# Kernel optimization log

Measured on AMD Instinct MI355X. Metric: run time of the kernel, lower is better.

## Reference

```python
import jax, jax.numpy as jnp
import numpy as np
import math

SEQ_LEN, PRED_LEN, CHANNELS, RANK = 720, 336, 862, 32
IN_LEN = SEQ_LEN // 2  # Haar low-pass with stride 2 (seq_len even)
BATCH = 256


def _dct2_ortho_mat(N):
    # D[k, n] = s_k * 2 * cos(pi * k * (2n+1) / (2N)); orthonormal DCT-II
    k = np.arange(N)[:, None]
    n = np.arange(N)[None, :]
    D = 2.0 * np.cos(np.pi * k * (2 * n + 1) / (2 * N))
    s = np.full(N, np.sqrt(1.0 / (2 * N)))
    s[0] = np.sqrt(1.0 / (4 * N))
    return jnp.asarray((s[:, None] * D).astype(np.float32))


def _idct2_unnorm_mat(N):
    # scipy.fft.idct(type=2, norm=None): out[n] = (1/N) * (x0/2 + sum_{k>=1} x_k cos(pi k (2n+1)/(2N)))
    # Returned as M[k, n] so that out = x @ M along last axis.
    k = np.arange(N)[:, None]
    n = np.arange(N)[None, :]
    M = np.cos(np.pi * k * (2 * n + 1) / (2 * N)) / N
    M[0, :] *= 0.5
    return jnp.asarray(M.astype(np.float32))


D_DCT = _dct2_ortho_mat(IN_LEN)        # [IN_LEN, IN_LEN]
M_IDCT = _idct2_unnorm_mat(PRED_LEN)   # [PRED_LEN, PRED_LEN]
INV_SQRT2 = 1.0 / math.sqrt(2.0)


def setup_inputs() -> dict:
    key = jax.random.key(0)
    k1, k2, k3, k4 = jax.random.split(key, 4)
    x = jax.random.normal(k1, (BATCH, SEQ_LEN, CHANNELS), dtype=jnp.float32)
    # kaiming_uniform-like scales for LowRank params
    boundA = math.sqrt(6.0 / IN_LEN)
    boundB = math.sqrt(6.0 / RANK)
    A = jax.random.uniform(k2, (IN_LEN, RANK), dtype=jnp.float32, minval=-boundA, maxval=boundA)
    B = jax.random.uniform(k3, (RANK, PRED_LEN), dtype=jnp.float32, minval=-boundB, maxval=boundB)
    b = jax.random.uniform(k4, (PRED_LEN,), dtype=jnp.float32)
    return {"x": x, "A": A, "B": B, "b": b}


def reference(x, A, B, b):
    # x: [B, L, C] -> [B, C, L]
    xt = jnp.transpose(x, (0, 2, 1))
    seq_mean = jnp.mean(xt, axis=-1, keepdims=True)          # [B, C, 1]
    xc = xt - seq_mean
    # Haar low-pass: depthwise conv1d with [1,1]/sqrt(2), stride 2
    h = (xc[..., ::2] + xc[..., 1::2]) * INV_SQRT2           # [B, C, IN_LEN]
    # orthonormal DCT-II along last axis, then divide by length
    y = jnp.einsum('bcn,kn->bck', h, D_DCT) / IN_LEN         # [B, C, IN_LEN]
    # low-rank prediction head (shared across channels)
    z = (y @ A) @ B + b                                      # [B, C, PRED_LEN]
    # unnormalized inverse DCT-II (scipy idct type=2, norm=None)
    o = z @ M_IDCT                                           # [B, C, PRED_LEN]
    o = o + seq_mean
    return jnp.transpose(o, (0, 2, 1))                       # [B, PRED_LEN, C]
```

## Files before the change

kernel.cpp:

```cpp
#include <hip/hip_runtime.h>
#include <math.h>

#define SEQ_LEN   720
#define IN_LEN    360
#define PRED_LEN  336
#define CHANNELS  862
#define RANK      32
#define BATCH     256

typedef _Float16 h2 __attribute__((ext_vector_type(2)));

#define WS_WP    0
#define WS_VT    11520
#define WS_CVEC  22272
#define WS_WH    22608
#define WS_VH    28368

__device__ __forceinline__ float fdot2w(h2 a, h2 b, float c) {
#if __has_builtin(__builtin_amdgcn_fdot2)
    return __builtin_amdgcn_fdot2(a, b, c, false);
#else
    return fmaf((float)a[0], (float)b[0], fmaf((float)a[1], (float)b[1], c));
#endif
}
__device__ __forceinline__ h2 pkrtz(float a, float b) {
    return __builtin_bit_cast(h2, __builtin_amdgcn_cvt_pkrtz(a, b));
}
#define BC(u) __builtin_bit_cast(h2, (u))

__global__ __launch_bounds__(256) void k_prep(const float* __restrict__ A,
                                              const float* __restrict__ B,
                                              const float* __restrict__ bias,
                                              float* __restrict__ Wp,
                                              float* __restrict__ Vt,
                                              float* __restrict__ cvec) {
    __shared__ float sbuf[IN_LEN * RANK];
    int blk = blockIdx.x;
    if (blk < 45) {
        for (int i = threadIdx.x; i < IN_LEN * RANK; i += 256) sbuf[i] = A[i];
        __syncthreads();
        int idx = blk * 256 + threadIdx.x;
        int n = idx >> 5, r = idx & 31;
        int step = 2 * n + 1, m = 0;
        float sum = 0.f;
        for (int k = 0; k < IN_LEN; ++k) {
            float coef = (k == 0) ? 0.05270462766947299f
                                  : 0.07453559924999299f;
            float d = coef * cospif((float)m * (1.0f / 720.0f));
            sum = fmaf(d, sbuf[k * RANK + r], sum);
            m += step; if (m >= 1440) m -= 1440;
        }
        Wp[idx] = sum * 0.0019641855032960957f;
    } else if (blk < 87) {
        for (int i = threadIdx.x; i < PRED_LEN * RANK; i += 256) {
            int r = i / PRED_LEN, k = i - r * PRED_LEN;
            sbuf[k * RANK + r] = B[i];
        }
        __syncthreads();
        int idx = (blk - 45) * 256 + threadIdx.x;
        int n = idx >> 5, r = idx & 31;
        int step = 2 * n + 1, m = 0;
        float sum = 0.f;
        for (int k = 0; k < PRED_LEN; ++k) {
            float mk = cospif((float)m * (1.0f / 672.0f));
            if (k == 0) mk *= 0.5f;
            sum = fmaf(mk, sbuf[k * RANK + r], sum);
            m += step; if (m >= 1344) m -= 1344;
        }
        Vt[idx] = sum * (1.0f / 336.0f);
    } else {
        int n = (blk - 87) * 256 + threadIdx.x;
        if (n < PRED_LEN) {
            int step = 2 * n + 1, m = 0;
            float sum = 0.f;
            for (int k = 0; k < PRED_LEN; ++k) {
                float mk = cospif((float)m * (1.0f / 672.0f));
                if (k == 0) mk *= 0.5f;
                sum = fmaf(mk, bias[k], sum);
                m += step; if (m >= 1344) m -= 1344;
            }
            cvec[n] = sum * (1.0f / 336.0f);
        }
    }
}

__global__ __launch_bounds__(256) void k_pack(const float* __restrict__ Wp,
                                              const float* __restrict__ Vt,
                                              unsigned* __restrict__ Wh,
                                              unsigned* __restrict__ Vh) {
    int idx = blockIdx.x * 256 + threadIdx.x;
    if (idx < 5760) {
        int np = idx >> 5, r = idx & 31;
        h2 v = pkrtz(Wp[(2 * np) * RANK + r], Wp[(2 * np + 1) * RANK + r]);
        Wh[idx] = __builtin_bit_cast(unsigned, v);
    } else if (idx < 5760 + 5376) {
        int j = idx - 5760;
        int n = j >> 4, q = j & 15;
        h2 v = pkrtz(Vt[n * RANK + 2 * q], Vt[n * RANK + 2 * q + 1]);
        Vh[j] = __builtin_bit_cast(unsigned, v);
    }
}

__global__ __launch_bounds__(448) void k_main(const float* __restrict__ x,
                                              const float* __restrict__ A,
                                              const unsigned* __restrict__ Wh,
                                              const unsigned* __restrict__ Vh,
                                              const float* __restrict__ cvec,
                                              float* __restrict__ out) {
    __shared__ uint4 lds4[2868];
    unsigned* ldsu = (unsigned*)lds4;
    const int tid = threadIdx.x;
    const int b = blockIdx.x;
    const int c0 = 2 * tid;
    const bool active = (tid < 431);

    for (int i = tid; i < 1440; i += 448) lds4[i] = ((const uint4*)Wh)[i];
    for (int i = tid; i < 1344; i += 448) lds4[1440 + i] = ((const uint4*)Vh)[i];
    for (int i = tid; i < PRED_LEN; i += 448) ldsu[11136 + i] = __float_as_uint(cvec[i]);
    __syncthreads();

    float acc0[RANK], acc1[RANK];
    #pragma unroll
    for (int r = 0; r < RANK; ++r) { acc0[r] = 0.f; acc1[r] = 0.f; }
    float S0 = 0.f, S1 = 0.f, mean0 = 0.f, mean1 = 0.f;
    h2 th0[16], th1[16];

    if (active) {
        const float* xp = x + (size_t)b * (SEQ_LEN * CHANNELS) + c0;

        float2 bufA[8], bufB[8];
        #define LOADB(BUF, BD) { const float* p_ = xp + (size_t)(BD) * (8 * CHANNELS); \
            _Pragma("unroll") \
            for (int j_ = 0; j_ < 8; ++j_) BUF[j_] = *(const float2*)(p_ + j_ * CHANNELS); }

        #define NPBODY(BUF, S_) { \
            float pe0 = BUF[4*S_+0].x + BUF[4*S_+1].x; \
            float pe1 = BUF[4*S_+0].y + BUF[4*S_+1].y; \
            float po0 = BUF[4*S_+2].x + BUF[4*S_+3].x; \
            float po1 = BUF[4*S_+2].y + BUF[4*S_+3].y; \
            S0 += pe0 + po0; S1 += pe1 + po1; \
            h2 P0 = pkrtz(pe0, po0); \
            h2 P1 = pkrtz(pe1, po1); \
            _Pragma("unroll") \
            for (int q_ = 0; q_ < 8; ++q_) { \
                uint4 wv = wr[8*S_ + q_]; \
                acc0[4*q_+0] = fdot2w(P0, BC(wv.x), acc0[4*q_+0]); \
                acc1[4*q_+0] = fdot2w(P1, BC(wv.x), acc1[4*q_+0]); \
                acc0[4*q_+1] = fdot2w(P0, BC(wv.y), acc0[4*q_+1]); \
                acc1[4*q_+1] = fdot2w(P1, BC(wv.y), acc1[4*q_+1]); \
                acc0[4*q_+2] = fdot2w(P0, BC(wv.z), acc0[4*q_+2]); \
                acc1[4*q_+2] = fdot2w(P1, BC(wv.z), acc1[4*q_+2]); \
                acc0[4*q_+3] = fdot2w(P0, BC(wv.w), acc0[4*q_+3]); \
                acc1[4*q_+3] = fdot2w(P1, BC(wv.w), acc1[4*q_+3]); \
            } }

        #define BODY(BUF, BD) { const uint4* wr = lds4 + 16 * (BD); \
            NPBODY(BUF, 0); NPBODY(BUF, 1); }

        LOADB(bufA, 0)
        for (int it = 0; it < 45; ++it) {
            LOADB(bufB, 2 * it + 1)
            BODY(bufA, 2 * it)
            if (it < 44) LOADB(bufA, 2 * it + 2)
            BODY(bufB, 2 * it + 1)
        }
        #undef BODY
        #undef NPBODY
        #undef LOADB

        const float k360 = (1.0f / 360.0f) * 0.037267799624996496f;
        float g0 = -S0 * k360, g1 = -S1 * k360;
        #pragma unroll
        for (int q = 0; q < 8; ++q) {
            float4 a4 = ((const float4*)A)[q];
            acc0[4*q+0] = fmaf(g0, a4.x, acc0[4*q+0]);
            acc1[4*q+0] = fmaf(g1, a4.x, acc1[4*q+0]);
            acc0[4*q+1] = fmaf(g0, a4.y, acc0[4*q+1]);
            acc1[4*q+1] = fmaf(g1, a4.y, acc1[4*q+1]);
            acc0[4*q+2] = fmaf(g0, a4.z, acc0[4*q+2]);
            acc1[4*q+2] = fmaf(g1, a4.z, acc1[4*q+2]);
            acc0[4*q+3] = fmaf(g0, a4.w, acc0[4*q+3]);
            acc1[4*q+3] = fmaf(g1, a4.w, acc1[4*q+3]);
        }
        mean0 = S0 * (1.0f / 720.0f);
        mean1 = S1 * (1.0f / 720.0f);

        #pragma unroll
        for (int u = 0; u < 16; ++u) {
            th0[u] = pkrtz(acc0[2*u], acc0[2*u+1]);
            th1[u] = pkrtz(acc1[2*u], acc1[2*u+1]);
        }

        float* op = out + (size_t)b * (PRED_LEN * CHANNELS) + c0;
        #pragma unroll 2
        for (int n = 0; n < PRED_LEN; ++n) {
            const uint4* vr = lds4 + 1440 + n * 4;
            float oA0 = 0.f, oB0 = 0.f, oA1 = 0.f, oB1 = 0.f;
            #pragma unroll
            for (int q = 0; q < 4; ++q) {
                uint4 v = vr[q];
                oA0 = fdot2w(th0[4*q+0], BC(v.x), oA0);
                oA1 = fdot2w(th1[4*q+0], BC(v.x), oA1);
                oB0 = fdot2w(th0[4*q+1], BC(v.y), oB0);
                oB1 = fdot2w(th1[4*q+1], BC(v.y), oB1);
                oA0 = fdot2w(th0[4*q+2], BC(v.z), oA0);
                oA1 = fdot2w(th1[4*q+2], BC(v.z), oA1);
                oB0 = fdot2w(th0[4*q+3], BC(v.w), oB0);
                oB1 = fdot2w(th1[4*q+3], BC(v.w), oB1);
            }
            float cvn = __uint_as_float(ldsu[11136 + n]);
            float2 o;
            o.x = (oA0 + oB0) + cvn + mean0;
            o.y = (oA1 + oB1) + cvn + mean1;
            *(float2*)op = o;
            op += CHANNELS;
        }
    }
}


extern "C" void kernel_launch(void* const* d_in, const int* in_sizes, int n_in,
                              void* d_out, int out_size, void* d_ws, size_t ws_size,
                              hipStream_t stream) {
    (void)in_sizes; (void)n_in; (void)out_size; (void)ws_size;
    const float* x    = (const float*)d_in[0];
    const float* A    = (const float*)d_in[1];
    const float* B    = (const float*)d_in[2];
    const float* bias = (const float*)d_in[3];
    float* out = (float*)d_out;
    float* ws  = (float*)d_ws;

    float*    Wp   = ws + WS_WP;
    float*    Vt   = ws + WS_VT;
    float*    cvec = ws + WS_CVEC;
    unsigned* Wh   = (unsigned*)(ws + WS_WH);
    unsigned* Vh   = (unsigned*)(ws + WS_VH);

    k_prep<<<dim3(89), dim3(256), 0, stream>>>(A, B, bias, Wp, Vt, cvec);
    k_pack<<<dim3(44), dim3(256), 0, stream>>>(Wp, Vt, Wh, Vh);
    k_main<<<dim3(BATCH), dim3(448), 0, stream>>>(x, A, Wh, Vh, cvec, out);
}
```

Before: 290.2 us.

## Split main kernel into sequence-half partial and prediction-half final kernels

Replaces the single per-batch kernel with two kernels. The first splits the sequence into two halves per batch, accumulating low-rank projections in packed fp16 FMA, and writes partial results and sums to workspace. The second combines the halves and computes the output for half of the prediction rows per block. This doubles the grid size, which should raise occupancy on a GPU that had only 256 blocks. In exchange it adds a workspace round-trip and an extra launch, and accumulating in fp16 instead of fp32 dot products reduces precision.

```diff
diff --git a/kernel.cpp b/kernel.cpp
--- a/kernel.cpp
+++ b/kernel.cpp
@@ -15,6 +15,8 @@
 #define WS_CVEC  22272
 #define WS_WH    22608
 #define WS_VH    28368
+#define WS_T     33744
+#define WS_S     7095248
 
 __device__ __forceinline__ float fdot2w(h2 a, h2 b, float c) {
 #if __has_builtin(__builtin_amdgcn_fdot2)
@@ -26,7 +28,8 @@
 __device__ __forceinline__ h2 pkrtz(float a, float b) {
     return __builtin_bit_cast(h2, __builtin_amdgcn_cvt_pkrtz(a, b));
 }
-#define BC(u) __builtin_bit_cast(h2, (u))
+#define BC(u)  __builtin_bit_cast(h2, (u))
+#define BCU(v) __builtin_bit_cast(unsigned, (v))
 
 __global__ __launch_bounds__(256) void k_prep(const float* __restrict__ A,
                                               const float* __restrict__ B,
@@ -90,131 +93,170 @@
                                               unsigned* __restrict__ Vh) {
     int idx = blockIdx.x * 256 + threadIdx.x;
     if (idx < 5760) {
-        int np = idx >> 5, r = idx & 31;
-        h2 v = pkrtz(Wp[(2 * np) * RANK + r], Wp[(2 * np + 1) * RANK + r]);
-        Wh[idx] = __builtin_bit_cast(unsigned, v);
+        int n = idx >> 4, j = idx & 15;
+        h2 v = pkrtz(Wp[n * RANK + 2 * j], Wp[n * RANK + 2 * j + 1]);
+        Wh[idx] = BCU(v);
     } else if (idx < 5760 + 5376) {
-        int j = idx - 5760;
-        int n = j >> 4, q = j & 15;
-        h2 v = pkrtz(Vt[n * RANK + 2 * q], Vt[n * RANK + 2 * q + 1]);
-        Vh[j] = __builtin_bit_cast(unsigned, v);
-    }
-}
-
-__global__ __launch_bounds__(448) void k_main(const float* __restrict__ x,
-                                              const float* __restrict__ A,
+        int k = idx - 5760;
+        int n = k >> 4, j = k & 15;
+        h2 v = pkrtz(Vt[n * RANK + 2 * j], Vt[n * RANK + 2 * j + 1]);
+        Vh[k] = BCU(v);
+    }
+}
+
+__global__ __launch_bounds__(512) void k_part(const float* __restrict__ x,
                                               const unsigned* __restrict__ Wh,
-                                              const unsigned* __restrict__ Vh,
-                                              const float* __restrict__ cvec,
-                                              float* __restrict__ out) {
-    __shared__ uint4 lds4[2868];
-    unsigned* ldsu = (unsigned*)lds4;
+                                              unsigned* __restrict__ wsT,
+                                              float* __restrict__ wsS) {
+    __shared__ uint4 lw4[720];
     const int tid = threadIdx.x;
-    const int b = blockIdx.x;
+    const int kh = blockIdx.x;
+    const int b  = blockIdx.y;
+
+    for (int i = tid; i < 720; i += 512)
+        lw4[i] = ((const uint4*)Wh)[kh * 720 + i];
+    __syncthreads();
+
     const int c0 = 2 * tid;
-    const bool active = (tid < 431);
-
-    for (int i = tid; i < 1440; i += 448) lds4[i] = ((const uint4*)Wh)[i];
-    for (int i = tid; i < 1344; i += 448) lds4[1440 + i] = ((const uint4*)Vh)[i];
-    for (int i = tid; i < PRED_LEN; i += 448) ldsu[11136 + i] = __float_as_uint(cvec[i]);
+    if (c0 >= CHANNELS) return;
+
+    h2 acc0[16], acc1[16];
+    #pragma unroll
+    for (int j = 0; j < 16; ++j) { acc0[j] = pkrtz(0.f, 0.f); acc1[j] = pkrtz(0.f, 0.f); }
+    float S0 = 0.f, S1 = 0.f;
+
+    const float* xp = x + (size_t)b * (SEQ_LEN * CHANNELS)
+                        + (size_t)kh * (IN_LEN * CHANNELS) + c0;
+
+    float2 bufA[8], bufB[8];
+    #define LOADB(BUF, CH) { const float* p_ = xp + (size_t)(CH) * (8 * CHANNELS); \
+        _Pragma("unroll") \
+        for (int j_ = 0; j_ < 8; ++j_) BUF[j_] = *(const float2*)(p_ + j_ * CHANNELS); }
+
+    #define BODY1(E, O, NL) { \
+        float p0 = E.x + O.x, p1 = E.y + O.y; \
+        S0 += p0; S1 += p1; \
+        h2 P0 = pkrtz(p0, p0), P1 = pkrtz(p1, p1); \
+        const uint4* wr = lw4 + (NL) * 4; \
+        _Pragma("unroll") \
+        for (int q_ = 0; q_ < 4; ++q_) { \
+            uint4 wv = wr[q_]; \
+            h2 w0 = BC(wv.x), w1 = BC(wv.y), w2 = BC(wv.z), w3 = BC(wv.w); \
+            acc0[4*q_+0] = w0 * P0 + acc0[4*q_+0]; \
+            acc1[4*q_+0] = w0 * P1 + acc1[4*q_+0]; \
+            acc0[4*q_+1] = w1 * P0 + acc0[4*q_+1]; \
+            acc1[4*q_+1] = w1 * P1 + acc1[4*q_+1]; \
+            acc0[4*q_+2] = w2 * P0 + acc0[4*q_+2]; \
+            acc1[4*q_+2] = w2 * P1 + acc1[4*q_+2]; \
+            acc0[4*q_+3] = w3 * P0 + acc0[4*q_+3]; \
+            acc1[4*q_+3] = w3 * P1 + acc1[4*q_+3]; \
+        } }
+
+    #define BODY4(BUF, NB) { \
+        BODY1(BUF[0], BUF[1], (NB) + 0) \
+        BODY1(BUF[2], BUF[3], (NB) + 1) \
+        BODY1(BUF[4], BUF[5], (NB) + 2) \
+        BODY1(BUF[6], BUF[7], (NB) + 3) }
+
+    LOADB(bufA, 0)
+    for (int it = 0; it < 22; ++it) {
+        LOADB(bufB, 2 * it + 1)
+        BODY4(bufA, 8 * it)
+        LOADB(bufA, 2 * it + 2)
+        BODY4(bufB, 8 * it + 4)
+    }
+    BODY4(bufA, 176)
+    #undef BODY4
+    #undef BODY1
+    #undef LOADB
+
+    uint4* r4 = (uint4*)(wsT + ((size_t)(kh * BATCH + b) * CHANNELS + c0) * 16);
+    #pragma unroll
+    for (int q = 0; q < 4; ++q) {
+        uint4 v;
+        v.x = BCU(acc0[4*q+0]); v.y = BCU(acc0[4*q+1]);
+        v.z = BCU(acc0[4*q+2]); v.w = BCU(acc0[4*q+3]);
+        r4[q] = v;
+        v.x = BCU(acc1[4*q+0]); v.y = BCU(acc1[4*q+1]);
+        v.z = BCU(acc1[4*q+2]); v.w = BCU(acc1[4*q+3]);
+        r4[4 + q] = v;
+    }
+    float2 sv; sv.x = S0; sv.y = S1;
+    *(float2*)(wsS + (size_t)(kh * BATCH + b) * CHANNELS + c0) = sv;
+}
+
+__global__ __launch_bounds__(512) void k_final(const float* __restrict__ A,
+                                               const unsigned* __restrict__ Vh,
+                                               const float* __restrict__ cvec,
+                                               const unsigned* __restrict__ wsT,
+                                               const float* __restrict__ wsS,
+                                               float* __restrict__ out) {
+    __shared__ uint4 lv4[672];
+    __shared__ float lcv[168];
+    const int tid = threadIdx.x;
+    const int nh = blockIdx.x;
+    const int b  = blockIdx.y;
+
+    for (int i = tid; i < 672; i += 512) lv4[i] = ((const uint4*)Vh)[nh * 672 + i];
+    for (int i = tid; i < 168; i += 512) lcv[i] = cvec[nh * 168 + i];
     __syncthreads();
 
-    float acc0[RANK], acc1[RANK];
-    #pragma unroll
-    for (int r = 0; r < RANK; ++r) { acc0[r] = 0.f; acc1[r] = 0.f; }
-    float S0 = 0.f, S1 = 0.f, mean0 = 0.f, mean1 = 0.f;
-    h2 th0[16], th1[16];
-
-    if (active) {
-        const float* xp = x + (size_t)b * (SEQ_LEN * CHANNELS) + c0;
-
-        float2 bufA[8], bufB[8];
-        #define LOADB(BUF, BD) { const float* p_ = xp + (size_t)(BD) * (8 * CHANNELS); \
-            _Pragma("unroll") \
-            for (int j_ = 0; j_ < 8; ++j_) BUF[j_] = *(const float2*)(p_ + j_ * CHANNELS); }
-
-        #define NPBODY(BUF, S_) { \
-            float pe0 = BUF[4*S_+0].x + BUF[4*S_+1].x; \
-            float pe1 = BUF[4*S_+0].y + BUF[4*S_+1].y; \
-            float po0 = BUF[4*S_+2].x + BUF[4*S_+3].x; \
-            float po1 = BUF[4*S_+2].y + BUF[4*S_+3].y; \
-            S0 += pe0 + po0; S1 += pe1 + po1; \
-            h2 P0 = pkrtz(pe0, po0); \
-            h2 P1 = pkrtz(pe1, po1); \
-            _Pragma("unroll") \
-            for (int q_ = 0; q_ < 8; ++q_) { \
-                uint4 wv = wr[8*S_ + q_]; \
-                acc0[4*q_+0] = fdot2w(P0, BC(wv.x), acc0[4*q_+0]); \
-                acc1[4*q_+0] = fdot2w(P1, BC(wv.x), acc1[4*q_+0]); \
-                acc0[4*q_+1] = fdot2w(P0, BC(wv.y), acc0[4*q_+1]); \
-                acc1[4*q_+1] = fdot2w(P1, BC(wv.y), acc1[4*q_+1]); \
-                acc0[4*q_+2] = fdot2w(P0, BC(wv.z), acc0[4*q_+2]); \
-                acc1[4*q_+2] = fdot2w(P1, BC(wv.z), acc1[4*q_+2]); \
-                acc0[4*q_+3] = fdot2w(P0, BC(wv.w), acc0[4*q_+3]); \
-                acc1[4*q_+3] = fdot2w(P1, BC(wv.w), acc1[4*q_+3]); \
-            } }
-
-        #define BODY(BUF, BD) { const uint4* wr = lds4 + 16 * (BD); \
-            NPBODY(BUF, 0); NPBODY(BUF, 1); }
-
-        LOADB(bufA, 0)
-        for (int it = 0; it < 45; ++it) {
-            LOADB(bufB, 2 * it + 1)
-            BODY(bufA, 2 * it)
-            if (it < 44) LOADB(bufA, 2 * it + 2)
-            BODY(bufB, 2 * it + 1)
-        }
-        #undef BODY
-        #undef NPBODY
-        #undef LOADB
-
-        const float k360 = (1.0f / 360.0f) * 0.037267799624996496f;
-        float g0 = -S0 * k360, g1 = -S1 * k360;
+    const int c0 = 2 * tid;
+    if (c0 >= CHANNELS) return;
+
+    const uint4* rA = (const uint4*)(wsT + ((size_t)(0 * BATCH + b) * CHANNELS + c0) * 16);
+    const uint4* rB = (const uint4*)(wsT + ((size_t)(1 * BATCH + b) * CHANNELS + c0) * 16);
+    h2 t0[16], t1[16];
+    #pragma unroll
+    for (int q = 0; q < 4; ++q) {
+        uint4 u = rA[q], v = rB[q];
+        t0[4*q+0] = BC(u.x) + BC(v.x); t0[4*q+1] = BC(u.y) + BC(v.y);
+        t0[4*q+2] = BC(u.z) + BC(v.z); t0[4*q+3] = BC(u.w) + BC(v.w);
+        u = rA[4 + q]; v = rB[4 + q];
+        t1[4*q+0] = BC(u.x) + BC(v.x); t1[4*q+1] = BC(u.y) + BC(v.y);
+        t1[4*q+2] = BC(u.z) + BC(v.z); t1[4*q+3] = BC(u.w) + BC(v.w);
+    }
+    float2 sA = *(const float2*)(wsS + (size_t)(0 * BATCH + b) * CHANNELS + c0);
+    float2 sB = *(const float2*)(wsS + (size_t)(1 * BATCH + b) * CHANNELS + c0);
+    float S0 = sA.x + sB.x, S1 = sA.y + sB.y;
+
+    const float kc = (1.0f / 360.0f) * 0.037267799624996496f;
+    float g0 = -S0 * kc, g1 = -S1 * kc;
+    h2 G0 = pkrtz(g0, g0), G1 = pkrtz(g1, g1);
+    #pragma unroll
+    for (int q = 0; q < 8; ++q) {
+        float4 a4 = ((const float4*)A)[q];
+        h2 aa = pkrtz(a4.x, a4.y), ab = pkrtz(a4.z, a4.w);
+        t0[2*q]   = aa * G0 + t0[2*q];   t0[2*q+1] = ab * G0 + t0[2*q+1];
+        t1[2*q]   = aa * G1 + t1[2*q];   t1[2*q+1] = ab * G1 + t1[2*q+1];
+    }
+    const float mean0 = S0 * (1.0f / 720.0f);
+    const float mean1 = S1 * (1.0f / 720.0f);
+
+    float* op = out + (size_t)b * (PRED_LEN * CHANNELS)
+                    + (size_t)(nh * 168) * CHANNELS + c0;
+    #pragma unroll 2
+    for (int nl = 0; nl < 168; ++nl) {
+        const uint4* vr = lv4 + nl * 4;
+        float oA0 = 0.f, oB0 = 0.f, oA1 = 0.f, oB1 = 0.f;
         #pragma unroll
-        for (int q = 0; q < 8; ++q) {
-            float4 a4 = ((const float4*)A)[q];
-            acc0[4*q+0] = fmaf(g0, a4.x, acc0[4*q+0]);
-            acc1[4*q+0] = fmaf(g1, a4.x, acc1[4*q+0]);
-            acc0[4*q+1] = fmaf(g0, a4.y, acc0[4*q+1]);
-            acc1[4*q+1] = fmaf(g1, a4.y, acc1[4*q+1]);
-            acc0[4*q+2] = fmaf(g0, a4.z, acc0[4*q+2]);
-            acc1[4*q+2] = fmaf(g1, a4.z, acc1[4*q+2]);
-            acc0[4*q+3] = fmaf(g0, a4.w, acc0[4*q+3]);
-            acc1[4*q+3] = fmaf(g1, a4.w, acc1[4*q+3]);
-        }
-        mean0 = S0 * (1.0f / 720.0f);
-        mean1 = S1 * (1.0f / 720.0f);
-
-        #pragma unroll
-        for (int u = 0; u < 16; ++u) {
-            th0[u] = pkrtz(acc0[2*u], acc0[2*u+1]);
-            th1[u] = pkrtz(acc1[2*u], acc1[2*u+1]);
-        }
-
-        float* op = out + (size_t)b * (PRED_LEN * CHANNELS) + c0;
-        #pragma unroll 2
-        for (int n = 0; n < PRED_LEN; ++n) {
-            const uint4* vr = lds4 + 1440 + n * 4;
-            float oA0 = 0.f, oB0 = 0.f, oA1 = 0.f, oB1 = 0.f;
-            #pragma unroll
-            for (int q = 0; q < 4; ++q) {
-                uint4 v = vr[q];
-                oA0 = fdot2w(th0[4*q+0], BC(v.x), oA0);
-                oA1 = fdot2w(th1[4*q+0], BC(v.x), oA1);
-                oB0 = fdot2w(th0[4*q+1], BC(v.y), oB0);
-                oB1 = fdot2w(th1[4*q+1], BC(v.y), oB1);
-                oA0 = fdot2w(th0[4*q+2], BC(v.z), oA0);
-                oA1 = fdot2w(th1[4*q+2], BC(v.z), oA1);
-                oB0 = fdot2w(th0[4*q+3], BC(v.w), oB0);
-                oB1 = fdot2w(th1[4*q+3], BC(v.w), oB1);
-            }
-            float cvn = __uint_as_float(ldsu[11136 + n]);
-            float2 o;
-            o.x = (oA0 + oB0) + cvn + mean0;
-            o.y = (oA1 + oB1) + cvn + mean1;
-            *(float2*)op = o;
-            op += CHANNELS;
-        }
+        for (int q = 0; q < 4; ++q) {
+            uint4 v = vr[q];
+            oA0 = fdot2w(t0[4*q+0], BC(v.x), oA0);
+            oA1 = fdot2w(t1[4*q+0], BC(v.x), oA1);
+            oB0 = fdot2w(t0[4*q+1], BC(v.y), oB0);
+            oB1 = fdot2w(t1[4*q+1], BC(v.y), oB1);
+            oA0 = fdot2w(t0[4*q+2], BC(v.z), oA0);
+            oA1 = fdot2w(t1[4*q+2], BC(v.z), oA1);
+            oB0 = fdot2w(t0[4*q+3], BC(v.w), oB0);
+            oB1 = fdot2w(t1[4*q+3], BC(v.w), oB1);
+        }
+        float cvn = lcv[nl];
+        float2 o;
+        o.x = (oA0 + oB0) + cvn + mean0;
+        o.y = (oA1 + oB1) + cvn + mean1;
+        *(float2*)op = o;
+        op += CHANNELS;
     }
 }
 
@@ -235,8 +277,11 @@
     float*    cvec = ws + WS_CVEC;
     unsigned* Wh   = (unsigned*)(ws + WS_WH);
     unsigned* Vh   = (unsigned*)(ws + WS_VH);
+    unsigned* wsT  = (unsigned*)(ws + WS_T);
+    float*    wsS  = ws + WS_S;
 
     k_prep<<<dim3(89), dim3(256), 0, stream>>>(A, B, bias, Wp, Vt, cvec);
     k_pack<<<dim3(44), dim3(256), 0, stream>>>(Wp, Vt, Wh, Vh);
-    k_main<<<dim3(BATCH), dim3(448), 0, stream>>>(x, A, Wh, Vh, cvec, out);
-}
+    k_part<<<dim3(2, BATCH), dim3(512), 0, stream>>>(x, Wh, wsT, wsS);
+    k_final<<<dim3(2, BATCH), dim3(512), 0, stream>>>(A, Vh, cvec, wsT, wsS, out);
+}
```

Result: slower. 309.1 us (+6.5%).
